# Performance work log

Hardware: AMD Instinct MI355X
Metric: run time of the kernel (lower is better)

The kernel has to match this reference:

```python
import jax, jax.numpy as jnp
import numpy as np
from functools import partial

FACTOR = 5
N_HEADS = 16


def setup_inputs() -> dict:
    key = jax.random.key(0)
    ks = jax.random.split(key, 8)
    B, L, D = 4, 4096, 1024
    scale = 0.02
    return {
        "q": jax.random.normal(ks[0], (B, L, D), jnp.float32),
        "k": jax.random.normal(ks[1], (B, L, D), jnp.float32),
        "v": jax.random.normal(ks[2], (B, L, D), jnp.float32),
        "Wq": jax.random.normal(ks[3], (D, D), jnp.float32) * scale,
        "bq": jnp.zeros((D,), jnp.float32),
        "Wk": jax.random.normal(ks[4], (D, D), jnp.float32) * scale,
        "bk": jnp.zeros((D,), jnp.float32),
        "Wv": jax.random.normal(ks[5], (D, D), jnp.float32) * scale,
        "bv": jnp.zeros((D,), jnp.float32),
        "Wo": jax.random.normal(ks[6], (D, D), jnp.float32) * scale,
        "bo": jnp.zeros((D,), jnp.float32),
    }


def _time_delay_agg(values, corr):
    # values, corr: (B, H, L, C).  Faithful to the repo: the double mean
    # over dim=1 reduces head then LENGTH, leaving (B, C); top-k indices
    # therefore live in [0, C) and are reused as time delays.
    B, H, L, C = values.shape
    top_k = int(FACTOR * np.log(L + 1)) if L > 1 else 1
    top_k = max(1, min(top_k, L))
    mean_value = corr.mean(axis=1).mean(axis=1)          # (B, C)
    mean_across_batch = mean_value.mean(axis=0)          # (C,)
    actual_k = min(top_k, C)
    _, indices = jax.lax.top_k(mean_across_batch, actual_k)  # (k,)
    selected = mean_value[:, indices]                    # (B, k)
    weights = jax.nn.softmax(selected, axis=-1)          # (B, k)
    t = jnp.arange(L)

    def body(acc, inp):
        d, w = inp                                       # scalar delay, (B,) weight
        idx = (t + d) % L                                # circular shift == roll of doubled tensor
        acc = acc + values[:, :, idx, :] * w[:, None, None, None]
        return acc, None

    agg, _ = jax.lax.scan(body, jnp.zeros_like(values), (indices, weights.T))
    return agg


def reference(q, k, v, Wq, bq, Wk, bk, Wv, bv, Wo, bo):
    B, L, D = q.shape
    H = N_HEADS
    dk = D // H

    def proj(x, W, b):
        y = x @ W.T + b
        return y.reshape(B, L, H, dk).transpose(0, 2, 1, 3)  # (B,H,L,dk)

    Q = proj(q, Wq, bq).astype(jnp.float32)
    K = proj(k, Wk, bk).astype(jnp.float32)
    V = proj(v, Wv, bv).astype(jnp.float32)

    Qf = jnp.fft.rfft(Q, axis=2)
    Kf = jnp.fft.rfft(K, axis=2)
    R = jnp.fft.irfft(Qf * jnp.conj(Kf), n=L, axis=2)    # (B,H,L,dk) autocorrelation

    V_agg = _time_delay_agg(V, R)                        # (B,H,L,dk)
    V_agg = V_agg.transpose(0, 2, 1, 3).reshape(B, L, D)
    return V_agg @ Wo.T + bo
```

## Files before the change

### kernel.cpp

```cpp
#include <hip/hip_runtime.h>
#include <hip/hip_bf16.h>

#define Bn 4
#define Ln 4096
#define Dn 1024
#define Hn 16
#define KSEL 41

typedef __attribute__((ext_vector_type(8))) _Float16 f16x8;
typedef __attribute__((ext_vector_type(4))) float f32x4;

__device__ __forceinline__ unsigned short f2h(float f) {
    union { _Float16 h; unsigned short u; } c;
    c.h = (_Float16)f;
    return c.u;
}

__device__ __forceinline__ void gl2lds16(const unsigned short* g, unsigned short* l) {
    __builtin_amdgcn_global_load_lds(
        (const __attribute__((address_space(1))) unsigned int*)(uintptr_t)g,
        (__attribute__((address_space(3))) unsigned int*)(uintptr_t)l,
        16, 0, 0);
}
__device__ __forceinline__ void gl2lds16f(const float* g, float* l) {
    __builtin_amdgcn_global_load_lds(
        (const __attribute__((address_space(1))) unsigned int*)(uintptr_t)g,
        (__attribute__((address_space(3))) unsigned int*)(uintptr_t)l,
        16, 0, 0);
}

__global__ __launch_bounds__(256) void colsum_part(const float* __restrict__ q,
                                                   const float* __restrict__ k,
                                                   float* __restrict__ part) {
    int tb = blockIdx.y; int tensor = tb >> 2, b = tb & 3;
    const f32x4* src = (const f32x4*)((tensor ? k : q) + (size_t)b * Ln * Dn) + threadIdx.x;
    int t0 = blockIdx.x * 128;
    f32x4 a0 = (f32x4){0.f, 0.f, 0.f, 0.f};
    f32x4 a1 = (f32x4){0.f, 0.f, 0.f, 0.f};
    #pragma unroll 1
    for (int g = 0; g < 16; ++g) {
        const f32x4* p = src + (size_t)(t0 + g * 8) * 256;
        f32x4 v0 = __builtin_nontemporal_load(p + 0 * 256);
        f32x4 v1 = __builtin_nontemporal_load(p + 1 * 256);
        f32x4 v2 = __builtin_nontemporal_load(p + 2 * 256);
        f32x4 v3 = __builtin_nontemporal_load(p + 3 * 256);
        f32x4 v4 = __builtin_nontemporal_load(p + 4 * 256);
        f32x4 v5 = __builtin_nontemporal_load(p + 5 * 256);
        f32x4 v6 = __builtin_nontemporal_load(p + 6 * 256);
        f32x4 v7 = __builtin_nontemporal_load(p + 7 * 256);
        a0 += v0 + v2 + v4 + v6;
        a1 += v1 + v3 + v5 + v7;
    }
    f32x4 o = a0 + a1;
    ((f32x4*)part)[((size_t)tb * 32 + blockIdx.x) * 256 + threadIdx.x] = o;
}

__global__ void colsum_fin(const float* __restrict__ part, float* __restrict__ sums) {
    int tb = blockIdx.y; int d = blockIdx.x * 256 + threadIdx.x;
    float s = 0.f;
    for (int i = 0; i < 32; ++i) s += part[((size_t)tb * 32 + i) * 1024 + d];
    sums[(size_t)tb * 1024 + d] = s;
}

__global__ void proj_sums(const float* __restrict__ sums,
                          const float* __restrict__ Wq, const float* __restrict__ bq,
                          const float* __restrict__ Wk, const float* __restrict__ bk,
                          float* __restrict__ SQK) {
    int t = blockIdx.y;
    const float* W    = t ? Wk : Wq;
    const float* bias = t ? bk : bq;
    const float* sv   = sums + (size_t)t * 4 * 1024;
    __shared__ float s_sv[4 * 1024];
    for (int i = threadIdx.x; i < 4 * 1024; i += 256) s_sv[i] = sv[i];
    __syncthreads();
    int wave = threadIdx.x >> 6, lane = threadIdx.x & 63;
    for (int rr = 0; rr < 4; ++rr) {
        int j = blockIdx.x * 16 + rr * 4 + wave;
        float p[4] = {0.f, 0.f, 0.f, 0.f};
        for (int c = 0; c < 4; ++c) {
            float4 wv = *(const float4*)(W + (size_t)j * 1024 + c * 256 + lane * 4);
            #pragma unroll
            for (int b = 0; b < 4; ++b) {
                float4 s = *(const float4*)(s_sv + b * 1024 + c * 256 + lane * 4);
                p[b] += wv.x * s.x + wv.y * s.y + wv.z * s.z + wv.w * s.w;
            }
        }
        #pragma unroll
        for (int b = 0; b < 4; ++b)
            for (int off = 1; off < 64; off <<= 1) p[b] += __shfl_xor(p[b], off);
        if (lane == 0) {
            float bb = bias[j] * (float)Ln;
            #pragma unroll
            for (int b = 0; b < 4; ++b) SQK[((size_t)t * 4 + b) * 1024 + j] = p[b] + bb;
        }
    }
}

__global__ void stats_topk(const float* __restrict__ SQK, int* __restrict__ dly,
                           float* __restrict__ gp) {
    __shared__ float s_mv[4][64];
    __shared__ float mab[64];
    __shared__ float selv[4][KSEL];
    __shared__ int   s_dly[KSEL];
    int tid = threadIdx.x; int b = tid >> 6, c = tid & 63;
    const float* SQ = SQK; const float* SK = SQK + 4 * 1024;
    float s = 0.f;
    for (int h = 0; h < Hn; ++h)
        s += SQ[(size_t)b * 1024 + h * 64 + c] * SK[(size_t)b * 1024 + h * 64 + c];
    s_mv[b][c] = s * (1.0f / ((float)Hn * (float)Ln));
    __syncthreads();
    if (tid < 64) mab[c] = (s_mv[0][c] + s_mv[1][c] + s_mv[2][c] + s_mv[3][c]) * 0.25f;
    __syncthreads();
    if (tid < 64) {
        float my = mab[c];
        int rank = 0;
        for (int j = 0; j < 64; ++j) {
            float vj = mab[j];
            rank += (vj > my) || (vj == my && j < c);
        }
        if (rank < KSEL) {
            s_dly[rank] = c;
            dly[rank] = c;
            selv[0][rank] = s_mv[0][c]; selv[1][rank] = s_mv[1][c];
            selv[2][rank] = s_mv[2][c]; selv[3][rank] = s_mv[3][c];
        }
    }
    __syncthreads();
    if (tid < 256) gp[tid] = 0.f;
    __syncthreads();
    if (tid < 4) {
        float mx = -1e30f;
        for (int i = 0; i < KSEL; ++i) mx = fmaxf(mx, selv[tid][i]);
        float ss = 0.f;
        for (int i = 0; i < KSEL; ++i) ss += expf(selv[tid][i] - mx);
        float inv = 1.0f / ss;
        for (int i = 0; i < KSEL; ++i)
            gp[tid * 64 + s_dly[i]] = expf(selv[tid][i] - mx) * inv;
    }
}

__global__ void prep_w(const float* __restrict__ Wo, const float* __restrict__ Wv,
                       unsigned short* __restrict__ Wof, unsigned short* __restrict__ WvTf) {
    int bx = blockIdx.x * 32, by = blockIdx.y * 32;
    int x = threadIdx.x, y0 = threadIdx.y;
    if (blockIdx.z == 0) {
        for (int i = 0; i < 32; i += 8) {
            size_t idx = (size_t)(by + y0 + i) * 1024 + bx + x;
            Wof[idx] = f2h(Wo[idx]);
        }
    } else {
        __shared__ float t[32][33];
        for (int i = 0; i < 32; i += 8)
            t[y0 + i][x] = Wv[(size_t)(by + y0 + i) * 1024 + bx + x];
        __syncthreads();
        for (int i = 0; i < 32; i += 8)
            WvTf[(size_t)(bx + y0 + i) * 1024 + by + x] = f2h(t[x][y0 + i]);
    }
}

__global__ void bcvec_k(const float* __restrict__ Wo, const float* __restrict__ bv,
                        const float* __restrict__ bo, float* __restrict__ bc) {
    __shared__ float s_bv[1024];
    for (int i = threadIdx.x; i < 1024; i += 256) s_bv[i] = bv[i];
    __syncthreads();
    int wave = threadIdx.x >> 6, lane = threadIdx.x & 63;
    for (int rr = 0; rr < 4; ++rr) {
        int n = blockIdx.x * 16 + rr * 4 + wave;
        float p = 0.f;
        for (int c = 0; c < 4; ++c) {
            float4 wv = *(const float4*)(Wo + (size_t)n * 1024 + c * 256 + lane * 4);
            float4 s  = *(const float4*)(s_bv + c * 256 + lane * 4);
            p += wv.x * s.x + wv.y * s.y + wv.z * s.z + wv.w * s.w;
        }
        for (int off = 1; off < 64; off <<= 1) p += __shfl_xor(p, off);
        if (lane == 0) bc[n] = p + bo[n];
    }
}

#define FT 128
#define FC 64
#define FW 64
__global__ __launch_bounds__(256) void gather_fir(const float* __restrict__ v,
                                                  const float* __restrict__ gp,
                                                  unsigned short* __restrict__ Vf) {
    __shared__ float S[(FT + FW) * FC];
    int b = blockIdx.z, c0 = blockIdx.y * FC, t0 = blockIdx.x * FT;
    const float* Vb = v + (size_t)b * Ln * Dn;
    #pragma unroll
    for (int it = 0; it < 12; ++it) {
        int idx = it * 256 + threadIdx.x;
        int r = idx >> 4, cc = idx & 15;
        int gr = (t0 + r) & (Ln - 1);
        gl2lds16f(Vb + (size_t)gr * Dn + c0 + cc * 4, S + idx * 4);
    }
    __syncthreads();
    int c4 = threadIdx.x & 15, rg = threadIdx.x >> 4;
    const int base = rg * 8;
    float4 acc[8];
    #pragma unroll
    for (int i = 0; i < 8; ++i) acc[i] = make_float4(0.f, 0.f, 0.f, 0.f);
    #pragma unroll
    for (int tc = 0; tc < 2; ++tc) {
        float gc[32];
        #pragma unroll
        for (int j = 0; j < 8; ++j) {
            float4 gv = ((const float4*)(gp + b * 64 + tc * 32))[j];
            gc[j * 4 + 0] = gv.x; gc[j * 4 + 1] = gv.y;
            gc[j * 4 + 2] = gv.z; gc[j * 4 + 3] = gv.w;
        }
        #pragma unroll
        for (int w = 0; w < 39; ++w) {
            float4 x = *(const float4*)&S[(base + tc * 32 + w) * FC + c4 * 4];
            #pragma unroll
            for (int i = 0; i < 8; ++i) {
                int j = w - i;
                if (j >= 0 && j < 32) {
                    float wt = gc[j];
                    acc[i].x += wt * x.x; acc[i].y += wt * x.y;
                    acc[i].z += wt * x.z; acc[i].w += wt * x.w;
                }
            }
        }
    }
    #pragma unroll
    for (int i = 0; i < 8; ++i) {
        size_t idx = ((size_t)b * Ln + t0 + base + i) * Dn + c0 + c4 * 4;
        ushort4 o;
        o.x = f2h(acc[i].x); o.y = f2h(acc[i].y);
        o.z = f2h(acc[i].z); o.w = f2h(acc[i].w);
        *(ushort4*)&Vf[idx] = o;
    }
}

template <int BM, bool OUT_F16>
__global__ __launch_bounds__(256, 2) void gemm_f16(
    const unsigned short* __restrict__ A, const unsigned short* __restrict__ Bt,
    float* __restrict__ C, unsigned short* __restrict__ Cf,
    const float* __restrict__ bias,
    int N, int K, int nbx) {
    constexpr int FM = BM / 32;
    __shared__ unsigned short sA[BM * 32];
    __shared__ unsigned short sB[BM * 32];

    int nwg = gridDim.x;
    int bid = blockIdx.x;
    int swz = (bid % 8) * (nwg / 8) + bid / 8;
    int by = swz / nbx, bx = swz % nbx;

    const int wave = threadIdx.x >> 6, lane = threadIdx.x & 63;
    const int lrow = lane & 15, lk = (lane >> 4) * 8;
    const int wr = wave >> 1, wc = wave & 1;

    f32x4 acc[FM][FM];
    #pragma unroll
    for (int i = 0; i < FM; ++i)
        #pragma unroll
        for (int j = 0; j < FM; ++j) acc[i][j] = (f32x4){0.f, 0.f, 0.f, 0.f};

    const int srow = lane >> 2;
    const int skq  = (lane & 3) * 8;

    for (int k0 = 0; k0 < K; k0 += 32) {
        #pragma unroll
        for (int j = 0; j < BM / 64; ++j) {
            int chunk = j * 4 + wave;
            int row = chunk * 16 + srow;
            gl2lds16(A  + (size_t)((by * BM) + row) * K + k0 + skq, sA + chunk * 512);
            gl2lds16(Bt + (size_t)((bx * BM) + row) * K + k0 + skq, sB + chunk * 512);
        }
        __syncthreads();
        f16x8 bfrag[FM];
        #pragma unroll
        for (int j = 0; j < FM; ++j) {
            int r = wc * (BM / 2) + j * 16 + lrow;
            bfrag[j] = *(const f16x8*)&sB[r * 32 + lk];
        }
        #pragma unroll
        for (int i = 0; i < FM; ++i) {
            int r = wr * (BM / 2) + i * 16 + lrow;
            f16x8 afrag = *(const f16x8*)&sA[r * 32 + lk];
            #pragma unroll
            for (int j = 0; j < FM; ++j)
                acc[i][j] = __builtin_amdgcn_mfma_f32_16x16x32_f16(afrag, bfrag[j], acc[i][j], 0, 0, 0);
        }
        __syncthreads();
    }
    #pragma unroll
    for (int i = 0; i < FM; ++i) {
        int r0 = by * BM + wr * (BM / 2) + i * 16 + (lane >> 4) * 4;
        #pragma unroll
        for (int j = 0; j < FM; ++j) {
            int c = bx * BM + wc * (BM / 2) + j * 16 + (lane & 15);
            float bb = OUT_F16 ? 0.f : bias[c];
            #pragma unroll
            for (int r = 0; r < 4; ++r) {
                size_t idx = (size_t)(r0 + r) * N + c;
                if (OUT_F16) Cf[idx] = f2h(acc[i][j][r]);
                else         C[idx]  = acc[i][j][r] + bb;
            }
        }
    }
}

extern "C" void kernel_launch(void* const* d_in, const int* in_sizes, int n_in,
                              void* d_out, int out_size, void* d_ws, size_t ws_size,
                              hipStream_t stream) {
    const float* q  = (const float*)d_in[0];
    const float* k  = (const float*)d_in[1];
    const float* v  = (const float*)d_in[2];
    const float* Wq = (const float*)d_in[3];
    const float* bq = (const float*)d_in[4];
    const float* Wk = (const float*)d_in[5];
    const float* bk = (const float*)d_in[6];
    const float* Wv = (const float*)d_in[7];
    const float* bv = (const float*)d_in[8];
    const float* Wo = (const float*)d_in[9];
    const float* bo = (const float*)d_in[10];
    float* out = (float*)d_out;
    float* ws  = (float*)d_ws;

    unsigned short* Vf    = (unsigned short*)ws;
    unsigned short* Wof   = Vf + 16777216;
    unsigned short* WvTf  = Wof + 1048576;
    unsigned short* Wcf   = WvTf + 1048576;
    float* part = (float*)(Wcf + 1048576);
    float* sums = part + 262144;
    float* SQK  = sums + 8192;
    float* gp   = SQK + 8192;
    float* bc   = gp + 256;
    int*   dly  = (int*)(bc + 1024);

    hipLaunchKernelGGL(colsum_part, dim3(32, 8), dim3(256), 0, stream, q, k, part);
    hipLaunchKernelGGL(colsum_fin, dim3(4, 8), dim3(256), 0, stream, part, sums);
    hipLaunchKernelGGL(proj_sums, dim3(64, 2), dim3(256), 0, stream, sums, Wq, bq, Wk, bk, SQK);
    hipLaunchKernelGGL(stats_topk, dim3(1), dim3(256), 0, stream, SQK, dly, gp);

    hipLaunchKernelGGL(prep_w, dim3(32, 32, 2), dim3(32, 8), 0, stream, Wo, Wv, Wof, WvTf);
    hipLaunchKernelGGL((gemm_f16<64, true>), dim3(256), dim3(256), 0, stream,
                       Wof, WvTf, (float*)nullptr, Wcf, (const float*)nullptr,
                       1024, 1024, 16);
    hipLaunchKernelGGL(bcvec_k, dim3(64), dim3(256), 0, stream, Wo, bv, bo, bc);

    hipLaunchKernelGGL(gather_fir, dim3(32, 16, 4), dim3(256), 0, stream, v, gp, Vf);

    hipLaunchKernelGGL((gemm_f16<128, false>), dim3(1024), dim3(256), 0, stream,
                       Vf, Wcf, out, (unsigned short*)nullptr, bc, 1024, 1024, 8);
}
```

Baseline: 138.7 us.

## Add 256x256-tile 8-wave pipelined GEMM and split colsum over more blocks

Replaces the final 128-tile f16 GEMM with a new 512-thread kernel that computes 256x256 output tiles as four 128x128 quadrants. It double-buffers the K-slices in LDS using direct global-to-LDS loads with an XOR swizzle, interleaves the staging of the next slices with MFMA work, and uses barriers and setprio to overlap loads with compute. Separately, the column-sum pass is split over twice as many blocks to improve occupancy, at the cost of a longer final reduction. The new GEMM uses 128 KB of LDS and many accumulators, which limits occupancy and adds register pressure.

Result: faster. 135.6 us (-2.2%).

```diff
diff --git a/kernel.cpp b/kernel.cpp
--- a/kernel.cpp
+++ b/kernel.cpp
@@ -6,6 +6,7 @@
 #define Dn 1024
 #define Hn 16
 #define KSEL 41
+#define NT8 16
 
 typedef __attribute__((ext_vector_type(8))) _Float16 f16x8;
 typedef __attribute__((ext_vector_type(4))) float f32x4;
@@ -34,11 +35,11 @@
                                                    float* __restrict__ part) {
     int tb = blockIdx.y; int tensor = tb >> 2, b = tb & 3;
     const f32x4* src = (const f32x4*)((tensor ? k : q) + (size_t)b * Ln * Dn) + threadIdx.x;
-    int t0 = blockIdx.x * 128;
+    int t0 = blockIdx.x * 64;
     f32x4 a0 = (f32x4){0.f, 0.f, 0.f, 0.f};
     f32x4 a1 = (f32x4){0.f, 0.f, 0.f, 0.f};
     #pragma unroll 1
-    for (int g = 0; g < 16; ++g) {
+    for (int g = 0; g < 8; ++g) {
         const f32x4* p = src + (size_t)(t0 + g * 8) * 256;
         f32x4 v0 = __builtin_nontemporal_load(p + 0 * 256);
         f32x4 v1 = __builtin_nontemporal_load(p + 1 * 256);
@@ -52,13 +53,13 @@
         a1 += v1 + v3 + v5 + v7;
     }
     f32x4 o = a0 + a1;
-    ((f32x4*)part)[((size_t)tb * 32 + blockIdx.x) * 256 + threadIdx.x] = o;
+    ((f32x4*)part)[((size_t)tb * 64 + blockIdx.x) * 256 + threadIdx.x] = o;
 }
 
 __global__ void colsum_fin(const float* __restrict__ part, float* __restrict__ sums) {
     int tb = blockIdx.y; int d = blockIdx.x * 256 + threadIdx.x;
     float s = 0.f;
-    for (int i = 0; i < 32; ++i) s += part[((size_t)tb * 32 + i) * 1024 + d];
+    for (int i = 0; i < 64; ++i) s += part[((size_t)tb * 64 + i) * 1024 + d];
     sums[(size_t)tb * 1024 + d] = s;
 }
 
@@ -298,6 +299,144 @@
                 if (OUT_F16) Cf[idx] = f2h(acc[i][j][r]);
                 else         C[idx]  = acc[i][j][r] + bb;
             }
+        }
+    }
+}
+
+__device__ __forceinline__ void mm16q(const f16x8* a, const f16x8* b, f32x4 (&acc)[2][4]) {
+    #pragma unroll
+    for (int i = 0; i < 2; ++i)
+        #pragma unroll
+        for (int j = 0; j < 4; ++j)
+            #pragma unroll
+            for (int s = 0; s < 2; ++s)
+                acc[i][j] = __builtin_amdgcn_mfma_f32_16x16x32_f16(a[i * 2 + s], b[j * 2 + s],
+                                                                   acc[i][j], 0, 0, 0);
+}
+
+__global__ __launch_bounds__(512, 2) void gemm8p(const unsigned short* __restrict__ A,
+                                                 const unsigned short* __restrict__ Bt,
+                                                 float* __restrict__ C,
+                                                 const float* __restrict__ bias) {
+    __shared__ unsigned short lds[65536];
+    int bid = blockIdx.x;
+    int swz = (bid & 7) * 32 + (bid >> 3);
+    int by = swz >> 2, bx = swz & 3;
+
+    const int tid = threadIdx.x;
+    const int wv = tid >> 6, lane = tid & 63;
+    const int wr = wv >> 1, wc = wv & 1;
+    const int srow = lane >> 3, sslot = lane & 7;
+
+    f32x4 acc[4][2][4];
+    #pragma unroll
+    for (int q = 0; q < 4; ++q)
+        #pragma unroll
+        for (int i = 0; i < 2; ++i)
+            #pragma unroll
+            for (int j = 0; j < 4; ++j) acc[q][i][j] = (f32x4){0.f, 0.f, 0.f, 0.f};
+
+    auto STAGE = [&](int t, int op, int mh) {
+        unsigned short* hb = lds + ((((t & 1) * 2 + op) * 2 + mh) << 13);
+        const unsigned short* G = op ? Bt : A;
+        int base_row = (op ? bx : by) * 256 + mh * 128;
+        #pragma unroll
+        for (int i = 0; i < 2; ++i) {
+            int rl = i * 64 + wv * 8 + srow;
+            int cs = sslot ^ (rl & 7);
+            gl2lds16(G + (size_t)(base_row + rl) * 1024 + t * 64 + cs * 8,
+                     hb + i * 4096 + wv * 512);
+        }
+    };
+    auto LDA = [&](int t, int h, f16x8* a) {
+        const unsigned short* hb = lds + ((((t & 1) * 2 + 0) * 2 + h) << 13);
+        #pragma unroll
+        for (int i = 0; i < 2; ++i) {
+            int rl = wr * 32 + i * 16 + (lane & 15);
+            #pragma unroll
+            for (int s = 0; s < 2; ++s) {
+                int cs = s * 4 + (lane >> 4);
+                a[i * 2 + s] = *(const f16x8*)(hb + rl * 64 + ((cs ^ (rl & 7)) << 3));
+            }
+        }
+    };
+    auto LDB = [&](int t, int h, f16x8* b) {
+        const unsigned short* hb = lds + ((((t & 1) * 2 + 1) * 2 + h) << 13);
+        #pragma unroll
+        for (int j = 0; j < 4; ++j) {
+            int rl = wc * 64 + j * 16 + (lane & 15);
+            #pragma unroll
+            for (int s = 0; s < 2; ++s) {
+                int cs = s * 4 + (lane >> 4);
+                b[j * 2 + s] = *(const f16x8*)(hb + rl * 64 + ((cs ^ (rl & 7)) << 3));
+            }
+        }
+    };
+
+    STAGE(0, 0, 0); STAGE(0, 1, 0); STAGE(0, 0, 1); STAGE(0, 1, 1);
+    STAGE(1, 0, 0); STAGE(1, 1, 0); STAGE(1, 0, 1);
+    asm volatile("s_waitcnt vmcnt(6)" ::: "memory");
+    __builtin_amdgcn_sched_barrier(0);
+    __builtin_amdgcn_s_barrier();
+
+    f16x8 a0[4], a1[4], b[8];
+    for (int t = 0; t < NT8; ++t) {
+        LDA(t, 0, a0); LDB(t, 0, b);
+        asm volatile("s_waitcnt lgkmcnt(0)" ::: "memory");
+        __builtin_amdgcn_sched_barrier(0);
+        __builtin_amdgcn_s_barrier();
+        __builtin_amdgcn_sched_barrier(0);
+        if (t + 1 < NT8) STAGE(t + 1, 1, 1);
+        __builtin_amdgcn_s_setprio(1);
+        mm16q(a0, b, acc[0]);
+        __builtin_amdgcn_s_setprio(0);
+        LDA(t, 1, a1);
+        asm volatile("s_waitcnt lgkmcnt(0)" ::: "memory");
+        __builtin_amdgcn_sched_barrier(0);
+        __builtin_amdgcn_s_barrier();
+        __builtin_amdgcn_sched_barrier(0);
+        if (t + 2 < NT8) STAGE(t + 2, 0, 0);
+        __builtin_amdgcn_s_setprio(1);
+        mm16q(a1, b, acc[2]);
+        __builtin_amdgcn_s_setprio(0);
+        LDB(t, 1, b);
+        asm volatile("s_waitcnt lgkmcnt(0)" ::: "memory");
+        __builtin_amdgcn_sched_barrier(0);
+        __builtin_amdgcn_s_barrier();
+        __builtin_amdgcn_sched_barrier(0);
+        if (t + 2 < NT8) STAGE(t + 2, 1, 0);
+        __builtin_amdgcn_s_setprio(1);
+        mm16q(a0, b, acc[1]);
+        __builtin_amdgcn_s_setprio(0);
+        __builtin_amdgcn_s_barrier();
+        __builtin_amdgcn_sched_barrier(0);
+        if (t + 2 < NT8) STAGE(t + 2, 0, 1);
+        __builtin_amdgcn_s_setprio(1);
+        mm16q(a1, b, acc[3]);
+        __builtin_amdgcn_s_setprio(0);
+        if (t + 2 < NT8) {
+            asm volatile("s_waitcnt vmcnt(6)" ::: "memory");
+        } else {
+            asm volatile("s_waitcnt vmcnt(0)" ::: "memory");
+        }
+        __builtin_amdgcn_sched_barrier(0);
+        __builtin_amdgcn_s_barrier();
+    }
+
+    const int lr = (lane >> 4) << 2, lc = lane & 15;
+    #pragma unroll
+    for (int q = 0; q < 4; ++q) {
+        int rbase = by * 256 + (q >> 1) * 128 + wr * 32 + lr;
+        int cbase = bx * 256 + (q & 1) * 128 + wc * 64 + lc;
+        #pragma unroll
+        for (int j = 0; j < 4; ++j) {
+            int c = cbase + j * 16;
+            float bb = bias[c];
+            #pragma unroll
+            for (int i = 0; i < 2; ++i)
+                #pragma unroll
+                for (int r = 0; r < 4; ++r)
+                    C[(size_t)(rbase + i * 16 + r) * 1024 + c] = acc[q][i][j][r] + bb;
         }
     }
 }
@@ -324,13 +463,13 @@
     unsigned short* WvTf  = Wof + 1048576;
     unsigned short* Wcf   = WvTf + 1048576;
     float* part = (float*)(Wcf + 1048576);
-    float* sums = part + 262144;
+    float* sums = part + 524288;
     float* SQK  = sums + 8192;
     float* gp   = SQK + 8192;
     float* bc   = gp + 256;
     int*   dly  = (int*)(bc + 1024);
 
-    hipLaunchKernelGGL(colsum_part, dim3(32, 8), dim3(256), 0, stream, q, k, part);
+    hipLaunchKernelGGL(colsum_part, dim3(64, 8), dim3(256), 0, stream, q, k, part);
     hipLaunchKernelGGL(colsum_fin, dim3(4, 8), dim3(256), 0, stream, part, sums);
     hipLaunchKernelGGL(proj_sums, dim3(64, 2), dim3(256), 0, stream, sums, Wq, bq, Wk, bk, SQK);
     hipLaunchKernelGGL(stats_topk, dim3(1), dim3(256), 0, stream, SQK, dly, gp);
@@ -343,6 +482,5 @@
 
     hipLaunchKernelGGL(gather_fir, dim3(32, 16, 4), dim3(256), 0, stream, v, gp, Vf);
 
-    hipLaunchKernelGGL((gemm_f16<128, false>), dim3(1024), dim3(256), 0, stream,
-                       Vf, Wcf, out, (unsigned short*)nullptr, bc, 1024, 1024, 8);
-}
+    hipLaunchKernelGGL(gemm8p, dim3(256), dim3(512), 0, stream, Vf, Wcf, out, bc);
+}
```
